# Kernel optimization log

Hardware: AMD Instinct MI355X
Metric: run time of the kernel (lower is better)

The kernel has to match this reference:

```python
import jax, jax.numpy as jnp
import numpy as np

N, E = 50000, 800000          # nodes, directed edges
F_IN = 80                     # 16 unique sensors * 5 features
H, C = 4, 96                  # num_heads, hidden_dim
D = H * C                     # 384 = concat output dim per GAT layer
NC = 20                       # n_classes = number of components
NEG_SLOPE = 0.2               # PyG GATv2Conv default negative_slope
EPS = 1e-5                    # LayerNorm eps


def layer_norm(x, g, b):
    mu = x.mean(-1, keepdims=True)
    var = x.var(-1, keepdims=True)
    return (x - mu) * jax.lax.rsqrt(var + EPS) * g + b


def gatv2(x, src, dst, Wsrc, Wdst, att, bias):
    # GATv2Conv (concat=True): e_ij = att . leaky_relu(Wsrc x_j + Wdst x_i),
    # alpha = segment-softmax over dst, out_i = sum_j alpha_ij * (Wsrc x_j)
    n = x.shape[0]
    xs = (x @ Wsrc).reshape(n, H, C)
    xd = (x @ Wdst).reshape(n, H, C)
    m = jax.nn.leaky_relu(xs[src] + xd[dst], NEG_SLOPE)      # [E,H,C]
    e = jnp.einsum('ehc,hc->eh', m, att)                     # [E,H]
    emax = jax.ops.segment_max(e, dst, num_segments=n)       # [N,H]
    ex = jnp.exp(e - emax[dst])
    denom = jax.ops.segment_sum(ex, dst, num_segments=n)
    alpha = ex / (denom[dst] + 1e-16)                        # [E,H]
    out = jax.ops.segment_sum(alpha[:, :, None] * xs[src], dst, num_segments=n)
    return out.reshape(n, D) + bias


def setup_inputs():
    key = jax.random.key(0)
    ks = jax.random.split(key, 16)

    def w(k, shape, fan):
        return (jax.random.normal(k, shape, jnp.float32) / np.float32(np.sqrt(fan)))

    inp = {
        'x': jax.random.normal(ks[0], (N, F_IN), jnp.float32),
        'edge_index': jax.random.randint(ks[1], (2, E), 0, N, jnp.int32),
    }
    dims = [F_IN, D, D]
    i = 2
    for l in range(3):
        inp[f'Wsrc{l}'] = w(ks[i], (dims[l], D), dims[l]); i += 1
        inp[f'Wdst{l}'] = w(ks[i], (dims[l], D), dims[l]); i += 1
        inp[f'att{l}'] = w(ks[i], (H, C), C); i += 1
        inp[f'b{l}'] = jnp.zeros((D,), jnp.float32)
        inp[f'g{l}'] = jnp.ones((D,), jnp.float32)
        inp[f'be{l}'] = jnp.zeros((D,), jnp.float32)
    inp['Wc1'] = w(ks[i], (D, C), D); i += 1
    inp['bc1'] = jnp.zeros((C,), jnp.float32)
    inp['gc'] = jnp.ones((C,), jnp.float32)
    inp['bec'] = jnp.zeros((C,), jnp.float32)
    inp['Wc2'] = w(ks[i], (C, NC), C)
    inp['bc2'] = jnp.zeros((NC,), jnp.float32)
    return inp


def reference(x, edge_index,
              Wsrc0, Wdst0, att0, b0, g0, be0,
              Wsrc1, Wdst1, att1, b1, g1, be1,
              Wsrc2, Wdst2, att2, b2, g2, be2,
              Wc1, bc1, gc, bec, Wc2, bc2):
    src, dst = edge_index[0], edge_index[1]
    layers = [(Wsrc0, Wdst0, att0, b0, g0, be0),
              (Wsrc1, Wdst1, att1, b1, g1, be1),
              (Wsrc2, Wdst2, att2, b2, g2, be2)]
    h = x
    for (Ws, Wd, a, b, g, be) in layers:
        h = gatv2(h, src, dst, Ws, Wd, a, b)
        h = jax.nn.elu(layer_norm(h, g, be))   # dropout: identity in eval mode
    h = jax.nn.relu(h @ Wc1 + bc1)
    h = layer_norm(h, gc, bec)
    return h @ Wc2 + bc2
```

## Files before the change

kernel.cpp:

```cpp
#include <hip/hip_runtime.h>
#include <math.h>

#define D 384
#define NCLS 20
#define FIN 80
#define CH 96

typedef unsigned int u32t;
typedef unsigned short u16t;
typedef __attribute__((ext_vector_type(8))) short bf16x8;
typedef __attribute__((ext_vector_type(4))) float f32x4;

__device__ __forceinline__ u16t f2bf(float f) {
    u32t b = __float_as_uint(f);
    u32t r = (b + 0x7FFFu + ((b >> 16) & 1u)) >> 16;
    return (u16t)r;
}
__device__ __forceinline__ float bfl(u32t u) { return __uint_as_float(u << 16); }
__device__ __forceinline__ float bfh(u32t u) { return __uint_as_float(u & 0xFFFF0000u); }

#define GLOAD16(g, l)                                                            \
    __builtin_amdgcn_global_load_lds(                                            \
        (const __attribute__((address_space(1))) void*)(g),                      \
        (__attribute__((address_space(3))) void*)(l), 16, 0, 0)


__global__ void k_zero(int* p, int n) {
    int i = blockIdx.x * blockDim.x + threadIdx.x;
    if (i < n) p[i] = 0;
}

__global__ void k_hist(const int* __restrict__ dst, int* __restrict__ deg, int E) {
    int i = blockIdx.x * blockDim.x + threadIdx.x;
    if (i < E) atomicAdd(&deg[dst[i]], 1);
}

__global__ __launch_bounds__(256) void k_scan1(const int* __restrict__ deg,
                                               int* __restrict__ offs,
                                               int* __restrict__ bsum, int n) {
    __shared__ int sh[256];
    int t = threadIdx.x, i = blockIdx.x * 256 + t;
    int v = (i < n) ? deg[i] : 0;
    sh[t] = v;
    __syncthreads();
    for (int o = 1; o < 256; o <<= 1) {
        int a = (t >= o) ? sh[t - o] : 0;
        __syncthreads();
        sh[t] += a;
        __syncthreads();
    }
    if (i < n) offs[i] = sh[t] - v;
    if (t == 255) bsum[blockIdx.x] = sh[255];
}

__global__ __launch_bounds__(256) void k_scan2(int* __restrict__ bsum, int nb,
                                               int* __restrict__ offs, int n) {
    __shared__ int sh[256];
    int t = threadIdx.x;
    int v = (t < nb) ? bsum[t] : 0;
    sh[t] = v;
    __syncthreads();
    for (int o = 1; o < 256; o <<= 1) {
        int a = (t >= o) ? sh[t - o] : 0;
        __syncthreads();
        sh[t] += a;
        __syncthreads();
    }
    if (t < nb) bsum[t] = sh[t] - v;
    if (t == 255) offs[n] = sh[255];
}

__global__ __launch_bounds__(256) void k_scan3(int* __restrict__ offs,
                                               int* __restrict__ cursor,
                                               const int* __restrict__ bsum, int n) {
    int i = blockIdx.x * 256 + threadIdx.x;
    if (i < n) {
        int o = offs[i] + bsum[blockIdx.x];
        offs[i] = o;
        cursor[i] = o;
    }
}

__global__ void k_scatter(const int* __restrict__ src, const int* __restrict__ dst,
                          int* __restrict__ cursor, int* __restrict__ csr_src, int E) {
    int i = blockIdx.x * blockDim.x + threadIdx.x;
    if (i < E) {
        int p = atomicAdd(&cursor[dst[i]], 1);
        csr_src[p] = src[i];
    }
}


__global__ void k_cvt_x(const float* __restrict__ x, u16t* __restrict__ xbf, int N) {
    int i = blockIdx.x * 256 + threadIdx.x;
    if (i >= N * 96) return;
    int r = i / 96, c = i - r * 96;
    float v = (c < FIN) ? x[r * FIN + c] : 0.f;
    xbf[i] = f2bf(v);
}

__global__ void k_cvt_wT(const float* __restrict__ W, u16t* __restrict__ WT,
                         int K, int Kp) {
    int i = blockIdx.x * 256 + threadIdx.x;
    if (i >= D * Kp) return;
    int c = i / Kp, k = i - c * Kp;
    float v = (k < K) ? W[(size_t)k * D + c] : 0.f;
    WT[i] = f2bf(v);
}

__global__ void k_cvt_wc1T(const float* __restrict__ W, u16t* __restrict__ WT) {
    int i = blockIdx.x * 256 + threadIdx.x;
    if (i >= 128 * D) return;
    int c = i / D, k = i - c * D;
    float v = (c < CH) ? W[(size_t)k * CH + c] : 0.f;
    WT[i] = f2bf(v);
}


__global__ __launch_bounds__(256) void k_mm(const u16t* __restrict__ A,
                                            const u16t* __restrict__ BT,
                                            u16t* __restrict__ C, int Kp) {
    __shared__ u16t Al[4][128][8];
    __shared__ u16t Bl[4][128][8];
    const int t = threadIdx.x;
    const int wave = t >> 6, lane = t & 63;
    const int wr = wave >> 1, wc = wave & 1;
    const int bm0 = blockIdx.x * 128;
    const int bn0 = blockIdx.y * 128;
    const int col16 = lane & 15, kc = lane >> 4;

    f32x4 acc[4][4] = {};

    const u16t* asrc0 = A + (size_t)(bm0 + lane) * Kp + wave * 8;
    const u16t* asrc1 = A + (size_t)(bm0 + 64 + lane) * Kp + wave * 8;
    const u16t* bsrc0 = BT + (size_t)(bn0 + lane) * Kp + wave * 8;
    const u16t* bsrc1 = BT + (size_t)(bn0 + 64 + lane) * Kp + wave * 8;
    u16t* alds0 = &Al[wave][0][0];
    u16t* alds1 = &Al[wave][64][0];
    u16t* blds0 = &Bl[wave][0][0];
    u16t* blds1 = &Bl[wave][64][0];

    for (int k0 = 0; k0 < Kp; k0 += 32) {
        GLOAD16(asrc0 + k0, alds0);
        GLOAD16(asrc1 + k0, alds1);
        GLOAD16(bsrc0 + k0, blds0);
        GLOAD16(bsrc1 + k0, blds1);
        __syncthreads();

        bf16x8 a[4], b[4];
#pragma unroll
        for (int m = 0; m < 4; m++)
            a[m] = *(const bf16x8*)&Al[kc][wr * 64 + m * 16 + col16][0];
#pragma unroll
        for (int n = 0; n < 4; n++)
            b[n] = *(const bf16x8*)&Bl[kc][wc * 64 + n * 16 + col16][0];
#pragma unroll
        for (int m = 0; m < 4; m++)
#pragma unroll
            for (int n = 0; n < 4; n++)
                acc[m][n] = __builtin_amdgcn_mfma_f32_16x16x32_bf16(
                    a[m], b[n], acc[m][n], 0, 0, 0);
        __syncthreads();
    }

#pragma unroll
    for (int m = 0; m < 4; m++) {
#pragma unroll
        for (int n = 0; n < 4; n++) {
#pragma unroll
            for (int j = 0; j < 4; j++) {
                int row = bm0 + wr * 64 + m * 16 + (lane >> 4) * 4 + j;
                int col = bn0 + wc * 64 + n * 16 + col16;
                C[(size_t)row * D + col] = f2bf(acc[m][n][j]);
            }
        }
    }
}


__global__ __launch_bounds__(256) void k_mmh(const u16t* __restrict__ A,
                                             const u16t* __restrict__ BT,
                                             const float* __restrict__ bc1,
                                             float* __restrict__ Yh) {
    __shared__ u16t Al[4][128][8];
    __shared__ u16t Bl[4][128][8];
    const int t = threadIdx.x;
    const int wave = t >> 6, lane = t & 63;
    const int wr = wave >> 1, wc = wave & 1;
    const int bm0 = blockIdx.x * 128;
    const int col16 = lane & 15, kc = lane >> 4;

    f32x4 acc[4][4] = {};

    const u16t* asrc0 = A + (size_t)(bm0 + lane) * D + wave * 8;
    const u16t* asrc1 = A + (size_t)(bm0 + 64 + lane) * D + wave * 8;
    const u16t* bsrc0 = BT + (size_t)lane * D + wave * 8;
    const u16t* bsrc1 = BT + (size_t)(64 + lane) * D + wave * 8;
    u16t* alds0 = &Al[wave][0][0];
    u16t* alds1 = &Al[wave][64][0];
    u16t* blds0 = &Bl[wave][0][0];
    u16t* blds1 = &Bl[wave][64][0];

    for (int k0 = 0; k0 < D; k0 += 32) {
        GLOAD16(asrc0 + k0, alds0);
        GLOAD16(asrc1 + k0, alds1);
        GLOAD16(bsrc0 + k0, blds0);
        GLOAD16(bsrc1 + k0, blds1);
        __syncthreads();

        bf16x8 a[4], b[4];
#pragma unroll
        for (int m = 0; m < 4; m++)
            a[m] = *(const bf16x8*)&Al[kc][wr * 64 + m * 16 + col16][0];
#pragma unroll
        for (int n = 0; n < 4; n++)
            b[n] = *(const bf16x8*)&Bl[kc][wc * 64 + n * 16 + col16][0];
#pragma unroll
        for (int m = 0; m < 4; m++)
#pragma unroll
            for (int n = 0; n < 4; n++)
                acc[m][n] = __builtin_amdgcn_mfma_f32_16x16x32_bf16(
                    a[m], b[n], acc[m][n], 0, 0, 0);
        __syncthreads();
    }

#pragma unroll
    for (int m = 0; m < 4; m++) {
#pragma unroll
        for (int n = 0; n < 4; n++) {
            int col = wc * 64 + n * 16 + col16;
            if (col < CH) {
                float bc = bc1[col];
#pragma unroll
                for (int j = 0; j < 4; j++) {
                    int row = bm0 + wr * 64 + m * 16 + (lane >> 4) * 4 + j;
                    Yh[(size_t)row * CH + col] = fmaxf(acc[m][n][j] + bc, 0.f);
                }
            }
        }
    }
}


__global__ __launch_bounds__(256) void k_gat(const u16t* __restrict__ XS,
                                             const u16t* __restrict__ XD,
                                             const float* __restrict__ att,
                                             const float* __restrict__ bias,
                                             const float* __restrict__ gamma,
                                             const float* __restrict__ beta,
                                             const int* __restrict__ offs,
                                             const int* __restrict__ csr_src,
                                             u16t* __restrict__ Hout,
                                             int N) {
    int wave = threadIdx.x >> 6;
    int lane = threadIdx.x & 63;
    int node = blockIdx.x * 4 + wave;
    if (node >= N) return;
    int c0 = lane * 6;

    const u32t* xdp = (const u32t*)XD + (size_t)node * 192 + lane * 3;
    u32t d0 = xdp[0], d1 = xdp[1], d2 = xdp[2];
    float xd[6] = {bfl(d0), bfh(d0), bfl(d1), bfh(d1), bfl(d2), bfh(d2)};
    float attr[6];
#pragma unroll
    for (int k = 0; k < 6; k++) attr[k] = att[c0 + k];

    float m = -INFINITY, denom = 0.f;
    float acc[6] = {0.f, 0.f, 0.f, 0.f, 0.f, 0.f};
    int e0 = offs[node], e1 = offs[node + 1];

    for (int e = e0; e < e1; e++) {
        int s = csr_src[e];
        const u32t* xsp = (const u32t*)XS + (size_t)s * 192 + lane * 3;
        u32t a0 = xsp[0], a1 = xsp[1], a2 = xsp[2];
        float xs[6] = {bfl(a0), bfh(a0), bfl(a1), bfh(a1), bfl(a2), bfh(a2)};
        float part = 0.f;
#pragma unroll
        for (int k = 0; k < 6; k++) {
            float v = xs[k] + xd[k];
            v = v > 0.f ? v : 0.2f * v;
            part += v * attr[k];
        }
#pragma unroll
        for (int o = 1; o < 16; o <<= 1) part += __shfl_xor(part, o, 64);
        float enew = part;
        float nm = fmaxf(m, enew);
        float r = expf(m - nm);
        float p = expf(enew - nm);
        denom = denom * r + p;
#pragma unroll
        for (int k = 0; k < 6; k++) acc[k] = acc[k] * r + p * xs[k];
        m = nm;
    }

    float inv = 1.f / (denom + 1e-16f);
    float v[6];
    float s1 = 0.f;
#pragma unroll
    for (int k = 0; k < 6; k++) { v[k] = acc[k] * inv + bias[c0 + k]; s1 += v[k]; }
#pragma unroll
    for (int o = 1; o < 64; o <<= 1) s1 += __shfl_xor(s1, o, 64);
    float mu = s1 * (1.f / 384.f);
    float s2 = 0.f;
#pragma unroll
    for (int k = 0; k < 6; k++) { float d = v[k] - mu; s2 += d * d; }
#pragma unroll
    for (int o = 1; o < 64; o <<= 1) s2 += __shfl_xor(s2, o, 64);
    float rstd = rsqrtf(s2 * (1.f / 384.f) + 1e-5f);

    float ov[6];
#pragma unroll
    for (int k = 0; k < 6; k++) {
        float y = (v[k] - mu) * rstd * gamma[c0 + k] + beta[c0 + k];
        ov[k] = y > 0.f ? y : expm1f(y);
    }
    u32t w0 = (u32t)f2bf(ov[0]) | ((u32t)f2bf(ov[1]) << 16);
    u32t w1 = (u32t)f2bf(ov[2]) | ((u32t)f2bf(ov[3]) << 16);
    u32t w2 = (u32t)f2bf(ov[4]) | ((u32t)f2bf(ov[5]) << 16);
    u32t* hp = (u32t*)Hout + (size_t)node * 192 + lane * 3;
    hp[0] = w0; hp[1] = w1; hp[2] = w2;
}


__global__ __launch_bounds__(256) void k_lnout(const float* __restrict__ Yh,
                                               const float* __restrict__ gc,
                                               const float* __restrict__ bec,
                                               const float* __restrict__ Wc2,
                                               const float* __restrict__ bc2,
                                               float* __restrict__ out, int N) {
    __shared__ float w2[CH * NCLS];
    __shared__ float ln[8][CH];
    int t = threadIdx.x;
    int g = t >> 5, tl = t & 31;
    int node = blockIdx.x * 8 + g;

    for (int i = t; i < CH * NCLS; i += 256) w2[i] = Wc2[i];

    if (node < N) {
        const float* yp = Yh + (size_t)node * CH;
        float y0 = yp[tl], y1 = yp[32 + tl], y2 = yp[64 + tl];
        float s = y0 + y1 + y2;
#pragma unroll
        for (int o = 1; o < 32; o <<= 1) s += __shfl_xor(s, o, 32);
        float mu = s * (1.f / CH);
        float d0 = y0 - mu, d1 = y1 - mu, d2 = y2 - mu;
        float q = d0 * d0 + d1 * d1 + d2 * d2;
#pragma unroll
        for (int o = 1; o < 32; o <<= 1) q += __shfl_xor(q, o, 32);
        float rstd = rsqrtf(q * (1.f / CH) + 1e-5f);
        ln[g][tl]      = d0 * rstd * gc[tl]      + bec[tl];
        ln[g][32 + tl] = d1 * rstd * gc[32 + tl] + bec[32 + tl];
        ln[g][64 + tl] = d2 * rstd * gc[64 + tl] + bec[64 + tl];
    }
    __syncthreads();

    if (node < N && tl < NCLS) {
        float o = bc2[tl];
        for (int c = 0; c < CH; c++) o += ln[g][c] * w2[c * NCLS + tl];
        out[(size_t)node * NCLS + tl] = o;
    }
}


extern "C" void kernel_launch(void* const* d_in, const int* in_sizes, int n_in,
                              void* d_out, int out_size, void* d_ws, size_t ws_size,
                              hipStream_t stream) {
    const float* x        = (const float*)d_in[0];
    const int*   eidx     = (const int*)d_in[1];
    const float* Wsrc[3]  = {(const float*)d_in[2],  (const float*)d_in[8],  (const float*)d_in[14]};
    const float* Wdst[3]  = {(const float*)d_in[3],  (const float*)d_in[9],  (const float*)d_in[15]};
    const float* attw[3]  = {(const float*)d_in[4],  (const float*)d_in[10], (const float*)d_in[16]};
    const float* bia[3]   = {(const float*)d_in[5],  (const float*)d_in[11], (const float*)d_in[17]};
    const float* gam[3]   = {(const float*)d_in[6],  (const float*)d_in[12], (const float*)d_in[18]};
    const float* bet[3]   = {(const float*)d_in[7],  (const float*)d_in[13], (const float*)d_in[19]};
    const float* Wc1 = (const float*)d_in[20];
    const float* bc1 = (const float*)d_in[21];
    const float* gc  = (const float*)d_in[22];
    const float* bec = (const float*)d_in[23];
    const float* Wc2 = (const float*)d_in[24];
    const float* bc2 = (const float*)d_in[25];

    const int N = in_sizes[0] / FIN;
    const int E = in_sizes[1] / 2;
    const int Mpad = ((N + 127) / 128) * 128;
    const int* srcp = eidx;
    const int* dstp = eidx + E;

    u16t* xbf  = (u16t*)d_ws;
    u16t* XSbf = xbf + (size_t)Mpad * 96;
    u16t* XDbf = XSbf + (size_t)Mpad * D;
    u16t* Hbf  = XDbf + (size_t)Mpad * D;
    u16t* WT0s = Hbf + (size_t)Mpad * D;
    u16t* WT0d = WT0s + 384 * 96;
    u16t* WT1s = WT0d + 384 * 96;
    u16t* WT1d = WT1s + 384 * 384;
    u16t* WT2s = WT1d + 384 * 384;
    u16t* WT2d = WT2s + 384 * 384;
    u16t* Wc1T = WT2d + 384 * 384;
    float* Yh  = (float*)(Wc1T + 128 * 384);
    int* offs    = (int*)(Yh + (size_t)Mpad * CH);
    int* cursor  = offs + (N + 1);
    int* deg     = cursor + (N + 1);
    int* bsum    = deg + N;
    int* csr_src = bsum + 512;

    const int nb = (N + 255) / 256;

    k_zero<<<nb, 256, 0, stream>>>(deg, N);
    k_hist<<<(E + 255) / 256, 256, 0, stream>>>(dstp, deg, E);
    k_scan1<<<nb, 256, 0, stream>>>(deg, offs, bsum, N);
    k_scan2<<<1, 256, 0, stream>>>(bsum, nb, offs, N);
    k_scan3<<<nb, 256, 0, stream>>>(offs, cursor, bsum, N);
    k_scatter<<<(E + 255) / 256, 256, 0, stream>>>(srcp, dstp, cursor, csr_src, E);

    k_cvt_x<<<(N * 96 + 255) / 256, 256, 0, stream>>>(x, xbf, N);
    k_cvt_wT<<<(D * 96 + 255) / 256, 256, 0, stream>>>(Wsrc[0], WT0s, FIN, 96);
    k_cvt_wT<<<(D * 96 + 255) / 256, 256, 0, stream>>>(Wdst[0], WT0d, FIN, 96);
    k_cvt_wT<<<(D * D + 255) / 256, 256, 0, stream>>>(Wsrc[1], WT1s, D, D);
    k_cvt_wT<<<(D * D + 255) / 256, 256, 0, stream>>>(Wdst[1], WT1d, D, D);
    k_cvt_wT<<<(D * D + 255) / 256, 256, 0, stream>>>(Wsrc[2], WT2s, D, D);
    k_cvt_wT<<<(D * D + 255) / 256, 256, 0, stream>>>(Wdst[2], WT2d, D, D);
    k_cvt_wc1T<<<(128 * D + 255) / 256, 256, 0, stream>>>(Wc1, Wc1T);

    dim3 gmm(Mpad / 128, D / 128);
    int gatGrid = (N + 3) / 4;

    k_mm<<<gmm, 256, 0, stream>>>(xbf, WT0s, XSbf, 96);
    k_mm<<<gmm, 256, 0, stream>>>(xbf, WT0d, XDbf, 96);
    k_gat<<<gatGrid, 256, 0, stream>>>(XSbf, XDbf, attw[0], bia[0], gam[0], bet[0],
                                       offs, csr_src, Hbf, N);
    k_mm<<<gmm, 256, 0, stream>>>(Hbf, WT1s, XSbf, D);
    k_mm<<<gmm, 256, 0, stream>>>(Hbf, WT1d, XDbf, D);
    k_gat<<<gatGrid, 256, 0, stream>>>(XSbf, XDbf, attw[1], bia[1], gam[1], bet[1],
                                       offs, csr_src, Hbf, N);
    k_mm<<<gmm, 256, 0, stream>>>(Hbf, WT2s, XSbf, D);
    k_mm<<<gmm, 256, 0, stream>>>(Hbf, WT2d, XDbf, D);
    k_gat<<<gatGrid, 256, 0, stream>>>(XSbf, XDbf, attw[2], bia[2], gam[2], bet[2],
                                       offs, csr_src, Hbf, N);

    k_mmh<<<Mpad / 128, 256, 0, stream>>>(Hbf, Wc1T, bc1, Yh);
    k_lnout<<<(N + 7) / 8, 256, 0, stream>>>(Yh, gc, bec, Wc2, bc2,
                                             (float*)d_out, N);
}
```

Before: 912.6 us.

## Fuse src/dst projection GEMMs into one interleaved output and lazily rescale softmax

The Wsrc and Wdst projections now run as a single GEMM with 768 output columns. This relies on the transposed weights already sitting next to each other in the workspace, and it writes XS and XD side by side in each node's row. The CSR source array stores the precomputed row offset, which drops a multiply from the gather loop. The GAT edge loop uses an online softmax that only rescales when a new score exceeds the running max by more than 8, and it uses fast __expf and fmaf. The goal is fewer kernel launches and a cheaper per-edge inner loop. The trade-off is that gathered XS rows are now strided by both halves, and the softmax precision changes slightly.

```diff
diff --git a/kernel.cpp b/kernel.cpp
--- a/kernel.cpp
+++ b/kernel.cpp
@@ -82,11 +82,11 @@
 }
 
 __global__ void k_scatter(const int* __restrict__ src, const int* __restrict__ dst,
-                          int* __restrict__ cursor, int* __restrict__ csr_src, int E) {
+                          int* __restrict__ cursor, int* __restrict__ csr_srcb, int E) {
     int i = blockIdx.x * blockDim.x + threadIdx.x;
     if (i < E) {
         int p = atomicAdd(&cursor[dst[i]], 1);
-        csr_src[p] = src[i];
+        csr_srcb[p] = src[i] * 384;
     }
 }
 
@@ -119,7 +119,7 @@
 
 __global__ __launch_bounds__(256) void k_mm(const u16t* __restrict__ A,
                                             const u16t* __restrict__ BT,
-                                            u16t* __restrict__ C, int Kp) {
+                                            u16t* __restrict__ C, int Kp, int ostride) {
     __shared__ u16t Al[4][128][8];
     __shared__ u16t Bl[4][128][8];
     const int t = threadIdx.x;
@@ -171,7 +171,7 @@
             for (int j = 0; j < 4; j++) {
                 int row = bm0 + wr * 64 + m * 16 + (lane >> 4) * 4 + j;
                 int col = bn0 + wc * 64 + n * 16 + col16;
-                C[(size_t)row * D + col] = f2bf(acc[m][n][j]);
+                C[(size_t)row * ostride + col] = f2bf(acc[m][n][j]);
             }
         }
     }
@@ -242,14 +242,13 @@
 }
 
 
-__global__ __launch_bounds__(256) void k_gat(const u16t* __restrict__ XS,
-                                             const u16t* __restrict__ XD,
+__global__ __launch_bounds__(256) void k_gat(const u32t* __restrict__ XSXD,
                                              const float* __restrict__ att,
                                              const float* __restrict__ bias,
                                              const float* __restrict__ gamma,
                                              const float* __restrict__ beta,
                                              const int* __restrict__ offs,
-                                             const int* __restrict__ csr_src,
+                                             const int* __restrict__ csr_srcb,
                                              u16t* __restrict__ Hout,
                                              int N) {
     int wave = threadIdx.x >> 6;
@@ -257,8 +256,9 @@
     int node = blockIdx.x * 4 + wave;
     if (node >= N) return;
     int c0 = lane * 6;
-
-    const u32t* xdp = (const u32t*)XD + (size_t)node * 192 + lane * 3;
+    int lo3 = lane * 3;
+
+    const u32t* xdp = XSXD + (size_t)node * 384 + 192 + lo3;
     u32t d0 = xdp[0], d1 = xdp[1], d2 = xdp[2];
     float xd[6] = {bfl(d0), bfh(d0), bfl(d1), bfh(d1), bfl(d2), bfh(d2)};
     float attr[6];
@@ -270,27 +270,32 @@
     int e0 = offs[node], e1 = offs[node + 1];
 
     for (int e = e0; e < e1; e++) {
-        int s = csr_src[e];
-        const u32t* xsp = (const u32t*)XS + (size_t)s * 192 + lane * 3;
+        const u32t* xsp = XSXD + (u32t)csr_srcb[e] + lo3;
         u32t a0 = xsp[0], a1 = xsp[1], a2 = xsp[2];
         float xs[6] = {bfl(a0), bfh(a0), bfl(a1), bfh(a1), bfl(a2), bfh(a2)};
         float part = 0.f;
 #pragma unroll
         for (int k = 0; k < 6; k++) {
             float v = xs[k] + xd[k];
-            v = v > 0.f ? v : 0.2f * v;
-            part += v * attr[k];
+            part = fmaf(fmaxf(v, 0.2f * v), attr[k], part);
         }
 #pragma unroll
         for (int o = 1; o < 16; o <<= 1) part += __shfl_xor(part, o, 64);
-        float enew = part;
-        float nm = fmaxf(m, enew);
-        float r = expf(m - nm);
-        float p = expf(enew - nm);
-        denom = denom * r + p;
-#pragma unroll
-        for (int k = 0; k < 6; k++) acc[k] = acc[k] * r + p * xs[k];
-        m = nm;
+
+        if (__builtin_expect(__any(part - m > 8.0f), 0)) {
+            float nm = fmaxf(m, part);
+            float r = __expf(m - nm);
+            float p = __expf(part - nm);
+            denom = denom * r + p;
+#pragma unroll
+            for (int k = 0; k < 6; k++) acc[k] = fmaf(p, xs[k], acc[k] * r);
+            m = nm;
+        } else {
+            float p = __expf(part - m);
+            denom += p;
+#pragma unroll
+            for (int k = 0; k < 6; k++) acc[k] = fmaf(p, xs[k], acc[k]);
+        }
     }
 
     float inv = 1.f / (denom + 1e-16f);
@@ -317,7 +322,7 @@
     u32t w0 = (u32t)f2bf(ov[0]) | ((u32t)f2bf(ov[1]) << 16);
     u32t w1 = (u32t)f2bf(ov[2]) | ((u32t)f2bf(ov[3]) << 16);
     u32t w2 = (u32t)f2bf(ov[4]) | ((u32t)f2bf(ov[5]) << 16);
-    u32t* hp = (u32t*)Hout + (size_t)node * 192 + lane * 3;
+    u32t* hp = (u32t*)Hout + (size_t)node * 192 + lo3;
     hp[0] = w0; hp[1] = w1; hp[2] = w2;
 }
 
@@ -387,9 +392,8 @@
     const int* dstp = eidx + E;
 
     u16t* xbf  = (u16t*)d_ws;
-    u16t* XSbf = xbf + (size_t)Mpad * 96;
-    u16t* XDbf = XSbf + (size_t)Mpad * D;
-    u16t* Hbf  = XDbf + (size_t)Mpad * D;
+    u16t* XSXD = xbf + (size_t)Mpad * 96;
+    u16t* Hbf  = XSXD + (size_t)Mpad * 768;
     u16t* WT0s = Hbf + (size_t)Mpad * D;
     u16t* WT0d = WT0s + 384 * 96;
     u16t* WT1s = WT0d + 384 * 96;
@@ -402,7 +406,7 @@
     int* cursor  = offs + (N + 1);
     int* deg     = cursor + (N + 1);
     int* bsum    = deg + N;
-    int* csr_src = bsum + 512;
+    int* csr_srcb = bsum + 512;
 
     const int nb = (N + 255) / 256;
 
@@ -411,7 +415,7 @@
     k_scan1<<<nb, 256, 0, stream>>>(deg, offs, bsum, N);
     k_scan2<<<1, 256, 0, stream>>>(bsum, nb, offs, N);
     k_scan3<<<nb, 256, 0, stream>>>(offs, cursor, bsum, N);
-    k_scatter<<<(E + 255) / 256, 256, 0, stream>>>(srcp, dstp, cursor, csr_src, E);
+    k_scatter<<<(E + 255) / 256, 256, 0, stream>>>(srcp, dstp, cursor, csr_srcb, E);
 
     k_cvt_x<<<(N * 96 + 255) / 256, 256, 0, stream>>>(x, xbf, N);
     k_cvt_wT<<<(D * 96 + 255) / 256, 256, 0, stream>>>(Wsrc[0], WT0s, FIN, 96);
@@ -422,21 +426,18 @@
     k_cvt_wT<<<(D * D + 255) / 256, 256, 0, stream>>>(Wdst[2], WT2d, D, D);
     k_cvt_wc1T<<<(128 * D + 255) / 256, 256, 0, stream>>>(Wc1, Wc1T);
 
-    dim3 gmm(Mpad / 128, D / 128);
+    dim3 gmm(Mpad / 128, 768 / 128);
     int gatGrid = (N + 3) / 4;
 
-    k_mm<<<gmm, 256, 0, stream>>>(xbf, WT0s, XSbf, 96);
-    k_mm<<<gmm, 256, 0, stream>>>(xbf, WT0d, XDbf, 96);
-    k_gat<<<gatGrid, 256, 0, stream>>>(XSbf, XDbf, attw[0], bia[0], gam[0], bet[0],
-                                       offs, csr_src, Hbf, N);
-    k_mm<<<gmm, 256, 0, stream>>>(Hbf, WT1s, XSbf, D);
-    k_mm<<<gmm, 256, 0, stream>>>(Hbf, WT1d, XDbf, D);
-    k_gat<<<gatGrid, 256, 0, stream>>>(XSbf, XDbf, attw[1], bia[1], gam[1], bet[1],
-                                       offs, csr_src, Hbf, N);
-    k_mm<<<gmm, 256, 0, stream>>>(Hbf, WT2s, XSbf, D);
-    k_mm<<<gmm, 256, 0, stream>>>(Hbf, WT2d, XDbf, D);
-    k_gat<<<gatGrid, 256, 0, stream>>>(XSbf, XDbf, attw[2], bia[2], gam[2], bet[2],
-                                       offs, csr_src, Hbf, N);
+    k_mm<<<gmm, 256, 0, stream>>>(xbf, WT0s, XSXD, 96, 768);
+    k_gat<<<gatGrid, 256, 0, stream>>>((const u32t*)XSXD, attw[0], bia[0], gam[0], bet[0],
+                                       offs, csr_srcb, Hbf, N);
+    k_mm<<<gmm, 256, 0, stream>>>(Hbf, WT1s, XSXD, D, 768);
+    k_gat<<<gatGrid, 256, 0, stream>>>((const u32t*)XSXD, attw[1], bia[1], gam[1], bet[1],
+                                       offs, csr_srcb, Hbf, N);
+    k_mm<<<gmm, 256, 0, stream>>>(Hbf, WT2s, XSXD, D, 768);
+    k_gat<<<gatGrid, 256, 0, stream>>>((const u32t*)XSXD, attw[2], bia[2], gam[2], bet[2],
+                                       offs, csr_srcb, Hbf, N);
 
     k_mmh<<<Mpad / 128, 256, 0, stream>>>(Hbf, Wc1T, bc1, Yh);
     k_lnout<<<(N + 7) / 8, 256, 0, stream>>>(Yh, gc, bec, Wc2, bc2,
```

New measurement: 865.5 us. 5.2% less time.
